# Kernel optimization log

Hardware: AMD Instinct MI355X
Metric: run time of the kernel (lower is better)

## Reference

```python
import jax, jax.numpy as jnp
import numpy as np

EPS = 1e-12  # matches F.normalize default eps


def _foolsgold(grads):
    # grads: [n, d]
    n = grads.shape[0]
    norm = jnp.maximum(jnp.linalg.norm(grads, axis=1, keepdims=True), EPS)
    normed = grads / norm
    eye = jnp.eye(n, dtype=grads.dtype)
    cs = normed @ normed.T - eye  # [n, n]
    maxcs = jnp.max(cs, axis=1)   # [n]
    # Vectorized form of: if i != j and maxcs[i] < maxcs[j]: cs[i,j] *= maxcs[i]/maxcs[j]
    mask = (maxcs[:, None] < maxcs[None, :]) & (eye == 0)
    cs = jnp.where(mask, cs * (maxcs[:, None] / maxcs[None, :]), cs)
    wv = 1.0 - jnp.max(cs, axis=1)
    wv = jnp.clip(wv, 0.0, 1.0)
    wv = wv / jnp.max(wv)
    wv = jnp.where(wv == 1.0, 0.99, wv)
    wv = jnp.log(wv / (1.0 - wv)) + 0.5
    # torch: wv[isinf(wv) + wv > 1] = 1  (bool + float, then > 1)
    wv = jnp.where(jnp.isinf(wv).astype(wv.dtype) + wv > 1.0, 1.0, wv)
    wv = jnp.where(wv < 0.0, 0.0, wv)
    return wv


def setup_inputs() -> dict:
    key = jax.random.key(0)
    d, n = 1000000, 100
    x = jax.random.normal(key, (1, d, n), dtype=jnp.float32)
    return {"input": x}


def reference(input) -> jnp.ndarray:
    x = input[0].T  # [n, d] per-client gradient vectors
    wv = _foolsgold(x)          # [n]
    w = wv / jnp.sum(wv)        # normalized client weights
    out = jnp.sum(x.T * w, axis=1, keepdims=True)  # [d, 1]
    return out
```

## Files before the change

### kernel.cpp

```cpp
#include <hip/hip_runtime.h>
#include <math.h>

#define NCLI 100
#define CPAD 112
#define DK   64
#define RAWB 28672
#define BFB  (CPAD * DK * 2)
#define GBLK 512

typedef short bf16x8 __attribute__((ext_vector_type(8)));
typedef float f32x4  __attribute__((ext_vector_type(4)));

__device__ __forceinline__ int bf_byte(int c, int t) {
    int s = (c & 7) ^ ((c >> 3) & 7);
    return c * 128 + ((t * 2) ^ (s << 4));
}

__device__ __forceinline__ unsigned short f2bf(float x) {
    unsigned u = __float_as_uint(x);
    unsigned r = (u + 0x7fffu + ((u >> 16) & 1u)) >> 16;
    return (unsigned short)r;
}

__global__ void zero_kernel(float4* __restrict__ p, int n4) {
    int i = blockIdx.x * blockDim.x + threadIdx.x;
    if (i < n4) p[i] = make_float4(0.f, 0.f, 0.f, 0.f);
}

__device__ __forceinline__ void stage_issue(const float* __restrict__ A, long c0,
                                            char* raw, int tid, long dtot) {
    const long gword0 = c0 * (DK * NCLI);
    const long gmax = dtot * NCLI - 4;
    const int wbyte = (tid & ~63) << 4;
#pragma unroll
    for (int i = 0; i < 7; ++i) {
        int f = i * 256 + tid;
        if (f > 1599) f = 1599;
        long gw = gword0 + (long)f * 4;
        if (gw > gmax) gw = gmax;
        __builtin_amdgcn_global_load_lds(
            (const __attribute__((address_space(1))) unsigned*)(A + gw),
            (__attribute__((address_space(3))) unsigned*)(raw + i * 4096 + wbyte),
            16, 0, 0);
    }
}

__device__ __forceinline__ void transpose_convert(const char* raw, char* bf,
                                                  int tid, long d0, long dtot) {
#pragma unroll
    for (int s = 0; s < 2; ++s) {
        if (s == 0 || tid < 144) {
            const int u = tid + s * 256;
            const int rg = u / 25;
            const int cg = u - rg * 25;
            float4 v[4];
#pragma unroll
            for (int r = 0; r < 4; ++r) {
                v[r] = *(const float4*)(raw + (((rg * 4 + r) * 25 + cg) << 4));
                if (d0 + rg * 4 + r >= dtot) v[r] = make_float4(0.f, 0.f, 0.f, 0.f);
            }
#pragma unroll
            for (int j = 0; j < 4; ++j) {
                const int c = cg * 4 + j;
                ushort4 p;
                p.x = f2bf(((const float*)&v[0])[j]);
                p.y = f2bf(((const float*)&v[1])[j]);
                p.z = f2bf(((const float*)&v[2])[j]);
                p.w = f2bf(((const float*)&v[3])[j]);
                *(ushort4*)(bf + bf_byte(c, rg * 4)) = p;
            }
        }
    }
}

template <int W>
__device__ __forceinline__ void compute_chunk(const char* bf, f32x4 acc[7]) {
    const int lane = threadIdx.x & 63;
    const int lrow = lane & 15;
    const int kgrp = lane >> 4;
    constexpr int NB = 7 - W;
#pragma unroll
    for (int kk = 0; kk < DK; kk += 32) {
        const int kb = kk + kgrp * 8;
        bf16x8 bfr[NB];
#pragma unroll
        for (int j = 0; j < NB; ++j)
            bfr[j] = *(const bf16x8*)(bf + bf_byte((W + j) * 16 + lrow, kb));
        bf16x8 a0 = *(const bf16x8*)(bf + bf_byte(W * 16 + lrow, kb));
#pragma unroll
        for (int j = 0; j < NB; ++j)
            acc[j] = __builtin_amdgcn_mfma_f32_16x16x32_bf16(a0, bfr[j], acc[j], 0, 0, 0);
        if constexpr (W > 0) {
            bf16x8 a1 = *(const bf16x8*)(bf + bf_byte((7 - W) * 16 + lrow, kb));
#pragma unroll
            for (int j = 0; j < W; ++j)
                acc[NB + j] = __builtin_amdgcn_mfma_f32_16x16x32_bf16(
                    a1, bfr[NB - W + j], acc[NB + j], 0, 0, 0);
        }
    }
}

template <int W>
__device__ __forceinline__ void store_acc(float* __restrict__ G, const f32x4 acc[7]) {
    const int lane = threadIdx.x & 63;
    const int cn = lane & 15;
    const int r0 = (lane >> 4) * 4;
#pragma unroll
    for (int j = 0; j < 7 - W; ++j) {
#pragma unroll
        for (int r = 0; r < 4; ++r) {
            int i = W * 16 + r0 + r;
            int k = (W + j) * 16 + cn;
            if (i < NCLI && k < NCLI) atomicAdd(&G[i * NCLI + k], acc[j][r]);
        }
    }
    if constexpr (W > 0) {
#pragma unroll
        for (int j = 0; j < W; ++j) {
#pragma unroll
            for (int r = 0; r < 4; ++r) {
                int i = (7 - W) * 16 + r0 + r;
                int k = (7 - W + j) * 16 + cn;
                if (i < NCLI && k < NCLI) atomicAdd(&G[i * NCLI + k], acc[7 - W + j][r]);
            }
        }
    }
}

__global__ __launch_bounds__(256, 2) void gram_mfma(const float* __restrict__ A,
                                                    float* __restrict__ G,
                                                    long dtot, int nchunks) {
    __shared__ char lds[2 * RAWB + BFB];
    char* bf = lds + 2 * RAWB;
    const int tid = threadIdx.x;
    const int wid = tid >> 6;

    for (int u = tid; u < (CPAD - NCLI) * 32; u += 256)
        ((unsigned*)(bf + NCLI * 128))[u] = 0u;
    __syncthreads();

    f32x4 acc[7];
#pragma unroll
    for (int q = 0; q < 7; ++q) acc[q] = (f32x4)(0.0f);

    int nb = 0;
    if ((int)blockIdx.x < nchunks)
        nb = (nchunks - 1 - (int)blockIdx.x) / (int)gridDim.x + 1;

    if (nb > 0)
        stage_issue(A, (long)blockIdx.x, lds, tid, dtot);

    for (int e = 0; e < nb; ++e) {
        char* raw_cur = lds + (e & 1) * RAWB;
        if (e + 1 < nb) {
            stage_issue(A, (long)blockIdx.x + (long)(e + 1) * gridDim.x,
                        lds + ((e + 1) & 1) * RAWB, tid, dtot);
            asm volatile("s_waitcnt vmcnt(7)" ::: "memory");
        } else {
            asm volatile("s_waitcnt vmcnt(0)" ::: "memory");
        }
        __builtin_amdgcn_s_barrier();
        asm volatile("" ::: "memory");

        transpose_convert(raw_cur, bf, tid,
                          ((long)blockIdx.x + (long)e * gridDim.x) * DK, dtot);

        asm volatile("s_waitcnt lgkmcnt(0)" ::: "memory");
        __builtin_amdgcn_s_barrier();
        asm volatile("" ::: "memory");

        if (wid == 0)      compute_chunk<0>(bf, acc);
        else if (wid == 1) compute_chunk<1>(bf, acc);
        else if (wid == 2) compute_chunk<2>(bf, acc);
        else               compute_chunk<3>(bf, acc);
    }

    if (wid == 0)      store_acc<0>(G, acc);
    else if (wid == 1) store_acc<1>(G, acc);
    else if (wid == 2) store_acc<2>(G, acc);
    else               store_acc<3>(G, acc);
}

__global__ __launch_bounds__(128) void weights_kernel(const float* __restrict__ G,
                                                      float* __restrict__ w) {
    __shared__ float cs[NCLI][NCLI + 1];
    __shared__ float nrm[NCLI], maxcs[NCLI], wv[NCLI];
    __shared__ float red[2];
    const int t = threadIdx.x;

    if (t < NCLI) {
        float g = G[t * NCLI + t];
        nrm[t] = fmaxf(sqrtf(g), 1e-12f);
    }
    __syncthreads();

    for (int idx = t; idx < NCLI * NCLI; idx += 128) {
        int i = idx / NCLI;
        int j = idx - i * NCLI;
        int a = i < j ? i : j;
        int b = i < j ? j : i;
        float c = G[a * NCLI + b] / (nrm[i] * nrm[j]);
        if (i == j) c -= 1.0f;
        cs[i][j] = c;
    }
    __syncthreads();

    if (t < NCLI) {
        float m = -1e30f;
        for (int j = 0; j < NCLI; ++j) m = fmaxf(m, cs[t][j]);
        maxcs[t] = m;
    }
    __syncthreads();

    if (t < NCLI) {
        float mi = maxcs[t];
        float m = -1e30f;
        for (int j = 0; j < NCLI; ++j) {
            float v = cs[t][j];
            float mj = maxcs[j];
            if (t != j && mi < mj) v *= mi / mj;
            m = fmaxf(m, v);
        }
        float x = 1.0f - m;
        x = fminf(fmaxf(x, 0.0f), 1.0f);
        wv[t] = x;
    }
    __syncthreads();

    if (t == 0) {
        float m = 0.0f;
        for (int i = 0; i < NCLI; ++i) m = fmaxf(m, wv[i]);
        red[0] = m;
    }
    __syncthreads();

    if (t < NCLI) {
        float x = wv[t] / red[0];
        if (x == 1.0f) x = 0.99f;
        float l = logf(x / (1.0f - x)) + 0.5f;
        float flag = isinf(l) ? 1.0f : 0.0f;
        l = (flag + l > 1.0f) ? 1.0f : l;
        l = (l < 0.0f) ? 0.0f : l;
        wv[t] = l;
    }
    __syncthreads();

    if (t == 0) {
        float s = 0.0f;
        for (int i = 0; i < NCLI; ++i) s += wv[i];
        red[1] = s;
    }
    __syncthreads();

    if (t < NCLI) w[t] = wv[t] / red[1];
}

__global__ __launch_bounds__(256) void out_kernel(const float* __restrict__ A,
                                                  const float* __restrict__ w,
                                                  float* __restrict__ out, int d,
                                                  int nblocks) {
    __shared__ float4 w4s[NCLI / 4];
    if (threadIdx.x < NCLI / 4) w4s[threadIdx.x] = ((const float4*)w)[threadIdx.x];
    __syncthreads();

    const int lane = threadIdx.x & 63;
    const int wid = threadIdx.x >> 6;
    const int q0 = lane & 3;
    const int rsub = lane >> 2;

    const long rb = (long)(nblocks - 1 - blockIdx.x) * 64;
    const long row = rb + wid * 16 + rsub;
    if (row >= d) return;

    const float4* r4 = (const float4*)(A + row * NCLI);
    float s = 0.0f;
#pragma unroll
    for (int k = 0; k < 6; ++k) {
        float4 v = r4[q0 + 4 * k];
        float4 ww = w4s[q0 + 4 * k];
        s += v.x * ww.x + v.y * ww.y + v.z * ww.z + v.w * ww.w;
    }
    if (q0 == 0) {
        float4 v = r4[24];
        float4 ww = w4s[24];
        s += v.x * ww.x + v.y * ww.y + v.z * ww.z + v.w * ww.w;
    }
    s += __shfl_xor(s, 1, 64);
    s += __shfl_xor(s, 2, 64);
    if (q0 == 0) out[row] = s;
}

extern "C" void kernel_launch(void* const* d_in, const int* in_sizes, int n_in,
                              void* d_out, int out_size, void* d_ws, size_t ws_size,
                              hipStream_t stream) {
    const float* A = (const float*)d_in[0];
    float* out = (float*)d_out;
    const int d = in_sizes[0] / NCLI;

    float* G = (float*)d_ws;
    float* w = G + NCLI * NCLI;

    const int n4 = (NCLI * NCLI) / 4;
    zero_kernel<<<(n4 + 255) / 256, 256, 0, stream>>>((float4*)G, n4);

    const int nchunks = (d + DK - 1) / DK;
    const int gblocks = nchunks < GBLK ? nchunks : GBLK;
    gram_mfma<<<gblocks, 256, 0, stream>>>(A, G, (long)d, nchunks);

    weights_kernel<<<1, 128, 0, stream>>>(G, w);

    const int oblocks = (d + 63) / 64;
    out_kernel<<<oblocks, 256, 0, stream>>>(A, w, out, d, oblocks);
}
```

Before: 200.8 us.

## Double-buffer bf16 tile and overlap MFMA compute with next transpose-convert

Result: no change. 199.1 us (-0.9%).

```diff
diff --git a/kernel.cpp b/kernel.cpp
--- a/kernel.cpp
+++ b/kernel.cpp
@@ -4,7 +4,7 @@
 #define NCLI 100
 #define CPAD 112
 #define DK   64
-#define RAWB 28672
+#define RAWB 25600
 #define BFB  (CPAD * DK * 2)
 #define GBLK 512
 
@@ -29,18 +29,26 @@
 
 __device__ __forceinline__ void stage_issue(const float* __restrict__ A, long c0,
                                             char* raw, int tid, long dtot) {
+    const int lane = tid & 63;
+    const int w = tid >> 6;
     const long gword0 = c0 * (DK * NCLI);
     const long gmax = dtot * NCLI - 4;
-    const int wbyte = (tid & ~63) << 4;
-#pragma unroll
-    for (int i = 0; i < 7; ++i) {
-        int f = i * 256 + tid;
-        if (f > 1599) f = 1599;
-        long gw = gword0 + (long)f * 4;
+#pragma unroll
+    for (int p = 0; p < 6; ++p) {
+        const int page = w * 6 + p;
+        long gw = gword0 + page * 256 + lane * 4;
         if (gw > gmax) gw = gmax;
         __builtin_amdgcn_global_load_lds(
             (const __attribute__((address_space(1))) unsigned*)(A + gw),
-            (__attribute__((address_space(3))) unsigned*)(raw + i * 4096 + wbyte),
+            (__attribute__((address_space(3))) unsigned*)(raw + page * 1024),
+            16, 0, 0);
+    }
+    if (w == 0) {
+        long gw = gword0 + 24 * 256 + lane * 4;
+        if (gw > gmax) gw = gmax;
+        __builtin_amdgcn_global_load_lds(
+            (const __attribute__((address_space(1))) unsigned*)(A + gw),
+            (__attribute__((address_space(3))) unsigned*)(raw + 24 * 1024),
             16, 0, 0);
     }
 }
@@ -130,13 +138,17 @@
 __global__ __launch_bounds__(256, 2) void gram_mfma(const float* __restrict__ A,
                                                     float* __restrict__ G,
                                                     long dtot, int nchunks) {
-    __shared__ char lds[2 * RAWB + BFB];
+    __shared__ uint4 ldsq[(2 * RAWB + 2 * BFB) / 16];
+    char* lds = (char*)ldsq;
     char* bf = lds + 2 * RAWB;
     const int tid = threadIdx.x;
     const int wid = tid >> 6;
 
-    for (int u = tid; u < (CPAD - NCLI) * 32; u += 256)
-        ((unsigned*)(bf + NCLI * 128))[u] = 0u;
+    for (int u = tid; u < 2 * (CPAD - NCLI) * 32; u += 256) {
+        int b = u / ((CPAD - NCLI) * 32);
+        int o = u - b * ((CPAD - NCLI) * 32);
+        ((unsigned*)(bf + b * BFB + NCLI * 128))[o] = 0u;
+    }
     __syncthreads();
 
     f32x4 acc[7];
@@ -151,28 +163,38 @@
         stage_issue(A, (long)blockIdx.x, lds, tid, dtot);
 
     for (int e = 0; e < nb; ++e) {
-        char* raw_cur = lds + (e & 1) * RAWB;
         if (e + 1 < nb) {
             stage_issue(A, (long)blockIdx.x + (long)(e + 1) * gridDim.x,
                         lds + ((e + 1) & 1) * RAWB, tid, dtot);
-            asm volatile("s_waitcnt vmcnt(7)" ::: "memory");
+            if (wid == 0) asm volatile("s_waitcnt vmcnt(7)" ::: "memory");
+            else          asm volatile("s_waitcnt vmcnt(6)" ::: "memory");
         } else {
             asm volatile("s_waitcnt vmcnt(0)" ::: "memory");
         }
         __builtin_amdgcn_s_barrier();
         asm volatile("" ::: "memory");
 
-        transpose_convert(raw_cur, bf, tid,
+        if (e > 0) {
+            const char* bfp = bf + ((e - 1) & 1) * BFB;
+            if (wid == 0)      compute_chunk<0>(bfp, acc);
+            else if (wid == 1) compute_chunk<1>(bfp, acc);
+            else if (wid == 2) compute_chunk<2>(bfp, acc);
+            else               compute_chunk<3>(bfp, acc);
+        }
+        transpose_convert(lds + (e & 1) * RAWB, bf + (e & 1) * BFB, tid,
                           ((long)blockIdx.x + (long)e * gridDim.x) * DK, dtot);
 
         asm volatile("s_waitcnt lgkmcnt(0)" ::: "memory");
         __builtin_amdgcn_s_barrier();
         asm volatile("" ::: "memory");
-
-        if (wid == 0)      compute_chunk<0>(bf, acc);
-        else if (wid == 1) compute_chunk<1>(bf, acc);
-        else if (wid == 2) compute_chunk<2>(bf, acc);
-        else               compute_chunk<3>(bf, acc);
+    }
+
+    if (nb > 0) {
+        const char* bfp = bf + ((nb - 1) & 1) * BFB;
+        if (wid == 0)      compute_chunk<0>(bfp, acc);
+        else if (wid == 1) compute_chunk<1>(bfp, acc);
+        else if (wid == 2) compute_chunk<2>(bfp, acc);
+        else               compute_chunk<3>(bfp, acc);
     }
 
     if (wid == 0)      store_acc<0>(G, acc);
```

## Replace LDS async staging with register prefetch and double-buffered bf16 tile

Applied to the files above, without the earlier changes.

Result: slower. 222.7 us (+10.9%).

```diff
diff --git a/kernel.cpp b/kernel.cpp
--- a/kernel.cpp
+++ b/kernel.cpp
@@ -4,9 +4,8 @@
 #define NCLI 100
 #define CPAD 112
 #define DK   64
-#define RAWB 28672
 #define BFB  (CPAD * DK * 2)
-#define GBLK 512
+#define GBLK 1024
 
 typedef short bf16x8 __attribute__((ext_vector_type(8)));
 typedef float f32x4  __attribute__((ext_vector_type(4)));
@@ -27,46 +26,39 @@
     if (i < n4) p[i] = make_float4(0.f, 0.f, 0.f, 0.f);
 }
 
-__device__ __forceinline__ void stage_issue(const float* __restrict__ A, long c0,
-                                            char* raw, int tid, long dtot) {
-    const long gword0 = c0 * (DK * NCLI);
-    const long gmax = dtot * NCLI - 4;
-    const int wbyte = (tid & ~63) << 4;
-#pragma unroll
-    for (int i = 0; i < 7; ++i) {
-        int f = i * 256 + tid;
-        if (f > 1599) f = 1599;
-        long gw = gword0 + (long)f * 4;
-        if (gw > gmax) gw = gmax;
-        __builtin_amdgcn_global_load_lds(
-            (const __attribute__((address_space(1))) unsigned*)(A + gw),
-            (__attribute__((address_space(3))) unsigned*)(raw + i * 4096 + wbyte),
-            16, 0, 0);
-    }
-}
-
-__device__ __forceinline__ void transpose_convert(const char* raw, char* bf,
-                                                  int tid, long d0, long dtot) {
+__device__ __forceinline__ void load_units(const float* __restrict__ A, long d0,
+                                           long dtot, int tid, float4 pv[2][4]) {
 #pragma unroll
     for (int s = 0; s < 2; ++s) {
         if (s == 0 || tid < 144) {
             const int u = tid + s * 256;
             const int rg = u / 25;
             const int cg = u - rg * 25;
-            float4 v[4];
 #pragma unroll
             for (int r = 0; r < 4; ++r) {
-                v[r] = *(const float4*)(raw + (((rg * 4 + r) * 25 + cg) << 4));
-                if (d0 + rg * 4 + r >= dtot) v[r] = make_float4(0.f, 0.f, 0.f, 0.f);
+                const long dr = d0 + rg * 4 + r;
+                pv[s][r] = (dr < dtot) ? *(const float4*)(A + dr * NCLI + cg * 4)
+                                       : make_float4(0.f, 0.f, 0.f, 0.f);
             }
+        }
+    }
+}
+
+__device__ __forceinline__ void write_units(char* bf, int tid, const float4 pv[2][4]) {
+#pragma unroll
+    for (int s = 0; s < 2; ++s) {
+        if (s == 0 || tid < 144) {
+            const int u = tid + s * 256;
+            const int rg = u / 25;
+            const int cg = u - rg * 25;
 #pragma unroll
             for (int j = 0; j < 4; ++j) {
                 const int c = cg * 4 + j;
                 ushort4 p;
-                p.x = f2bf(((const float*)&v[0])[j]);
-                p.y = f2bf(((const float*)&v[1])[j]);
-                p.z = f2bf(((const float*)&v[2])[j]);
-                p.w = f2bf(((const float*)&v[3])[j]);
+                p.x = f2bf(((const float*)&pv[s][0])[j]);
+                p.y = f2bf(((const float*)&pv[s][1])[j]);
+                p.z = f2bf(((const float*)&pv[s][2])[j]);
+                p.w = f2bf(((const float*)&pv[s][3])[j]);
                 *(ushort4*)(bf + bf_byte(c, rg * 4)) = p;
             }
         }
@@ -127,16 +119,19 @@
     }
 }
 
-__global__ __launch_bounds__(256, 2) void gram_mfma(const float* __restrict__ A,
+__global__ __launch_bounds__(256, 3) void gram_mfma(const float* __restrict__ A,
                                                     float* __restrict__ G,
                                                     long dtot, int nchunks) {
-    __shared__ char lds[2 * RAWB + BFB];
-    char* bf = lds + 2 * RAWB;
+    __shared__ uint4 ldsq[2 * BFB / 16];
+    char* bf = (char*)ldsq;
     const int tid = threadIdx.x;
     const int wid = tid >> 6;
 
-    for (int u = tid; u < (CPAD - NCLI) * 32; u += 256)
-        ((unsigned*)(bf + NCLI * 128))[u] = 0u;
+    for (int u = tid; u < 2 * (CPAD - NCLI) * 32; u += 256) {
+        int b = u / ((CPAD - NCLI) * 32);
+        int o = u - b * ((CPAD - NCLI) * 32);
+        ((unsigned*)(bf + b * BFB + NCLI * 128))[o] = 0u;
+    }
     __syncthreads();
 
     f32x4 acc[7];
@@ -147,32 +142,24 @@
     if ((int)blockIdx.x < nchunks)
         nb = (nchunks - 1 - (int)blockIdx.x) / (int)gridDim.x + 1;
 
+    float4 pv[2][4];
     if (nb > 0)
-        stage_issue(A, (long)blockIdx.x, lds, tid, dtot);
+        load_units(A, (long)blockIdx.x * DK, dtot, tid, pv);
 
     for (int e = 0; e < nb; ++e) {
-        char* raw_cur = lds + (e & 1) * RAWB;
-        if (e + 1 < nb) {
-            stage_issue(A, (long)blockIdx.x + (long)(e + 1) * gridDim.x,
-                        lds + ((e + 1) & 1) * RAWB, tid, dtot);
-            asm volatile("s_waitcnt vmcnt(7)" ::: "memory");
-        } else {
-            asm volatile("s_waitcnt vmcnt(0)" ::: "memory");
-        }
-        __builtin_amdgcn_s_barrier();
-        asm volatile("" ::: "memory");
-
-        transpose_convert(raw_cur, bf, tid,
-                          ((long)blockIdx.x + (long)e * gridDim.x) * DK, dtot);
-
+        char* bfc = bf + (e & 1) * BFB;
+        write_units(bfc, tid, pv);
+        if (e + 1 < nb)
+            load_units(A, ((long)blockIdx.x + (long)(e + 1) * gridDim.x) * DK,
+                       dtot, tid, pv);
         asm volatile("s_waitcnt lgkmcnt(0)" ::: "memory");
         __builtin_amdgcn_s_barrier();
         asm volatile("" ::: "memory");
 
-        if (wid == 0)      compute_chunk<0>(bf, acc);
-        else if (wid == 1) compute_chunk<1>(bf, acc);
-        else if (wid == 2) compute_chunk<2>(bf, acc);
-        else               compute_chunk<3>(bf, acc);
+        if (wid == 0)      compute_chunk<0>(bfc, acc);
+        else if (wid == 1) compute_chunk<1>(bfc, acc);
+        else if (wid == 2) compute_chunk<2>(bfc, acc);
+        else               compute_chunk<3>(bfc, acc);
     }
 
     if (wid == 0)      store_acc<0>(G, acc);
```
